# Kernel optimization log

Measured on AMD Instinct MI355X. Metric: run time of the kernel, lower is better.

## Reference

```python
import jax, jax.numpy as jnp
import numpy as np

B, DIM, HEADS, H, W = 4, 192, 6, 256, 256
C = DIM // HEADS  # channels per head
DN = ('NCHW', 'OIHW', 'NCHW')


def conv2d(x, w, b, padding='VALID', groups=1):
    y = jax.lax.conv_general_dilated(x, w, (1, 1), padding,
                                     dimension_numbers=DN,
                                     feature_group_count=groups)
    return y + b[None, :, None, None]


def setup_inputs() -> dict:
    key = jax.random.key(0)
    ks = jax.random.split(key, 8)
    s = 0.02
    return {
        'x': jax.random.normal(ks[0], (B, DIM, H, W), jnp.float32),
        'qkv_w': jax.random.normal(ks[1], (3 * DIM, DIM, 1, 1), jnp.float32) * s,
        'qkv_b': jnp.zeros((3 * DIM,), jnp.float32),
        'dw_w': jax.random.normal(ks[2], (3 * DIM, 1, 3, 3), jnp.float32) * s,
        'dw_b': jnp.zeros((3 * DIM,), jnp.float32),
        'proj_w': jax.random.normal(ks[3], (DIM, DIM, 1, 1), jnp.float32) * s,
        'proj_b': jnp.zeros((DIM,), jnp.float32),
        'temperature': jnp.ones((HEADS, 1, 1, 1), jnp.float32),
    }


def reference(x, qkv_w, qkv_b, dw_w, dw_b, proj_w, proj_b, temperature):
    # qkv projection: 1x1 conv then 3x3 depthwise conv
    qkv = conv2d(x, qkv_w, qkv_b)
    qkv = conv2d(qkv, dw_w, dw_b, padding='SAME', groups=3 * DIM)
    q, k, v = jnp.split(qkv, 3, axis=1)  # each (B, DIM, H, W)

    def heads(t):
        return t.reshape(B, HEADS, C, H, W)
    q, k, v = heads(q), heads(k), heads(v)

    # L2-normalize along W (matches F.normalize eps=1e-12)
    eps = 1e-12
    q = q / jnp.maximum(jnp.linalg.norm(q, axis=-1, keepdims=True), eps)
    k = k / jnp.maximum(jnp.linalg.norm(k, axis=-1, keepdims=True), eps)

    # per-channel HxH attention, contraction over W; temperature broadcasts over head
    attn = jnp.einsum('bncxw,bncyw->bncxy', q, k) * temperature  # (B,HEADS,C,H,H)
    attn = jax.nn.softmax(attn, axis=-1)
    out = jnp.einsum('bncxy,bncyw->bncxw', attn, v)  # (B,HEADS,C,H,W)

    out = out.reshape(B, DIM, H, W)
    return conv2d(out, proj_w, proj_b)
```

## Files before the change

kernel.cpp:

```cpp
#include <hip/hip_runtime.h>
#include <hip/hip_bf16.h>
#include <math.h>


#define HW 65536
#define IMW 256

typedef short bf16x8 __attribute__((ext_vector_type(8)));
typedef float f32x4  __attribute__((ext_vector_type(4)));

__device__ __forceinline__ float bf2f(ushort u) {
    return __uint_as_float((uint)u << 16);
}
__device__ __forceinline__ ushort f2bf(float f) {
    uint i = __float_as_uint(f);
    return (ushort)((i + 0x7FFFu + ((i >> 16) & 1u)) >> 16);
}

__global__ __launch_bounds__(256) void cvt_f32_bf16(const float* __restrict__ s,
                                                    ushort* __restrict__ d, int n)
{
    int i = blockIdx.x * 256 + threadIdx.x;
    if (i < n) d[i] = f2bf(s[i]);
}

__global__ __launch_bounds__(256) void cvt_transpose_f32(const float* __restrict__ src,
                                                         ushort* __restrict__ dst,
                                                         int R, int C,
                                                         long ssS, long ssD)
{
    __shared__ ushort Ls[64][72];
    int t = threadIdx.x;
    long z = blockIdx.z;
    src += z * ssS; dst += z * ssD;
    int c0 = blockIdx.x * 64, r0 = blockIdx.y * 64;
    {
        int r = t >> 2, cs = t & 3;
        const float* gp = src + (size_t)(r0 + r) * C + c0 + cs * 16;
        ushort tmp[16];
        #pragma unroll
        for (int q = 0; q < 4; ++q) {
            float4 v = *(const float4*)(gp + q * 4);
            tmp[q*4+0] = f2bf(v.x); tmp[q*4+1] = f2bf(v.y);
            tmp[q*4+2] = f2bf(v.z); tmp[q*4+3] = f2bf(v.w);
        }
        *(uint4*)&Ls[r][cs * 16]     = *(uint4*)&tmp[0];
        *(uint4*)&Ls[r][cs * 16 + 8] = *(uint4*)&tmp[8];
    }
    __syncthreads();
    {
        int cc = t & 63, seg = t >> 6;
        ushort tmp[16];
        #pragma unroll
        for (int j = 0; j < 16; ++j) tmp[j] = Ls[seg * 16 + j][cc];
        ushort* op = dst + (size_t)(c0 + cc) * R + r0 + seg * 16;
        *(uint4*)(op)     = *(uint4*)&tmp[0];
        *(uint4*)(op + 8) = *(uint4*)&tmp[8];
    }
}

__global__ __launch_bounds__(256) void transpose_bf16(const ushort* __restrict__ src,
                                                      ushort* __restrict__ dst,
                                                      int R, int C,
                                                      long ssS, long ssD)
{
    __shared__ ushort Ls[64][72];
    int t = threadIdx.x;
    long z = blockIdx.z;
    src += z * ssS; dst += z * ssD;
    int c0 = blockIdx.x * 64, r0 = blockIdx.y * 64;
    {
        int r = t >> 2, cs = t & 3;
        const ushort* gp = src + (size_t)(r0 + r) * C + c0 + cs * 16;
        *(uint4*)&Ls[r][cs * 16]     = *(const uint4*)(gp);
        *(uint4*)&Ls[r][cs * 16 + 8] = *(const uint4*)(gp + 8);
    }
    __syncthreads();
    {
        int cc = t & 63, seg = t >> 6;
        ushort tmp[16];
        #pragma unroll
        for (int j = 0; j < 16; ++j) tmp[j] = Ls[seg * 16 + j][cc];
        ushort* op = dst + (size_t)(c0 + cc) * R + r0 + seg * 16;
        *(uint4*)(op)     = *(uint4*)&tmp[0];
        *(uint4*)(op + 8) = *(uint4*)&tmp[8];
    }
}

__global__ __launch_bounds__(256) void transpose_v(const ushort* __restrict__ post,
                                                   ushort* __restrict__ vt)
{
    __shared__ ushort Ls[64][72];
    int t = threadIdx.x;
    int s = blockIdx.z;
    int b = s / 192, r = s - b * 192;
    const ushort* src = post + ((size_t)b * 576 + 384 + r) * HW;
    ushort*       dst = vt + (size_t)s * HW;
    int c0 = blockIdx.x * 64, r0 = blockIdx.y * 64;
    {
        int rr = t >> 2, cs = t & 3;
        const ushort* gp = src + (size_t)(r0 + rr) * IMW + c0 + cs * 16;
        *(uint4*)&Ls[rr][cs * 16]     = *(const uint4*)(gp);
        *(uint4*)&Ls[rr][cs * 16 + 8] = *(const uint4*)(gp + 8);
    }
    __syncthreads();
    {
        int cc = t & 63, seg = t >> 6;
        ushort tmp[16];
        #pragma unroll
        for (int j = 0; j < 16; ++j) tmp[j] = Ls[seg * 16 + j][cc];
        ushort* op = dst + (size_t)(c0 + cc) * IMW + r0 + seg * 16;
        *(uint4*)(op)     = *(uint4*)&tmp[0];
        *(uint4*)(op + 8) = *(uint4*)&tmp[8];
    }
}

__global__ __launch_bounds__(256) void gemm_mfma(const ushort* __restrict__ A, int lda, long sliceA,
                                                 const ushort* __restrict__ B, int ldb, long sliceB,
                                                 void* __restrict__ Dp, int ldd, long sliceD,
                                                 const float* __restrict__ bias,
                                                 int K, int outF32, int NM, int NN)
{
    int lin = blockIdx.x;
    int r8 = lin & 7, kk_ = lin >> 3;
    int m = kk_ % NM, fg = kk_ / NM;
    int g = fg * 8 + r8;
    int nt_ = g % NN;
    long z = g / NN;
    int m0 = m * 64, n0 = nt_ * 256;

    __shared__ ushort Ws[64][40];
    __shared__ ushort Xs[256][40];
    int t = threadIdx.x, wv = t >> 6, lane = t & 63;
    A += z * sliceA; B += z * sliceB;

    f32x4 acc[16];
    #pragma unroll
    for (int i = 0; i < 16; ++i) acc[i] = (f32x4){0.f, 0.f, 0.f, 0.f};

    for (int k0 = 0; k0 < K; k0 += 32) {
        {   int r = t >> 2, s = t & 3;
            *(uint4*)&Ws[r][s * 8] =
                *(const uint4*)(A + (size_t)(m0 + r) * lda + k0 + s * 8);
        }
        {   const ushort* bp = B + (size_t)(n0 + t) * ldb + k0;
            #pragma unroll
            for (int s = 0; s < 4; ++s)
                *(uint4*)&Xs[t][s * 8] = *(const uint4*)(bp + s * 8);
        }
        __syncthreads();
        bf16x8 a = *(const bf16x8*)&Ws[wv * 16 + (lane & 15)][(lane >> 4) * 8];
        #pragma unroll
        for (int nt = 0; nt < 16; ++nt) {
            bf16x8 b = *(const bf16x8*)&Xs[nt * 16 + (lane & 15)][(lane >> 4) * 8];
            acc[nt] = __builtin_amdgcn_mfma_f32_16x16x32_bf16(a, b, acc[nt], 0, 0, 0);
        }
        __syncthreads();
    }

    int mrow = m0 + wv * 16 + (lane >> 4) * 4;
    int ncol = n0 + (lane & 15);
    if (outF32) {
        float* D = (float*)Dp + z * sliceD;
        #pragma unroll
        for (int r_ = 0; r_ < 4; ++r_) {
            float bv = bias ? bias[mrow + r_] : 0.f;
            #pragma unroll
            for (int nt = 0; nt < 16; ++nt)
                D[(size_t)(mrow + r_) * ldd + ncol + nt * 16] = acc[nt][r_] + bv;
        }
    } else {
        ushort* D = (ushort*)Dp + z * sliceD;
        #pragma unroll
        for (int r_ = 0; r_ < 4; ++r_) {
            float bv = bias ? bias[mrow + r_] : 0.f;
            #pragma unroll
            for (int nt = 0; nt < 16; ++nt)
                D[(size_t)(mrow + r_) * ldd + ncol + nt * 16] = f2bf(acc[nt][r_] + bv);
        }
    }
}

__global__ __launch_bounds__(256) void attn_fused(const ushort* __restrict__ post,
                                                  const ushort* __restrict__ vt,
                                                  const float* __restrict__ temp,
                                                  ushort* __restrict__ O)
{
    __shared__ ushort Ws[64][40];
    __shared__ ushort Xs[256][40];
    __shared__ ushort Ps[64][264];
    int t = threadIdx.x, wv = t >> 6, lane = t & 63;
    int lin = blockIdx.x;
    int r8 = lin & 7, k_ = lin >> 3;
    int mtile = k_ & 3, fg = k_ >> 2;
    int s = fg * 8 + r8;
    int b = s / 192, ch = s - b * 192;
    const ushort* Aq = post + ((size_t)b * 576 + ch) * HW;
    const ushort* Bk = Aq + (size_t)192 * HW;
    const ushort* Vt = vt + (size_t)s * HW;
    int m0 = mtile * 64;

    f32x4 acc[16];
    #pragma unroll
    for (int i = 0; i < 16; ++i) acc[i] = (f32x4){0.f, 0.f, 0.f, 0.f};

    for (int k0 = 0; k0 < 256; k0 += 32) {
        {   int r = t >> 2, ss = t & 3;
            *(uint4*)&Ws[r][ss * 8] =
                *(const uint4*)(Aq + (size_t)(m0 + r) * IMW + k0 + ss * 8);
        }
        {   const ushort* bp = Bk + (size_t)t * IMW + k0;
            #pragma unroll
            for (int ss = 0; ss < 4; ++ss)
                *(uint4*)&Xs[t][ss * 8] = *(const uint4*)(bp + ss * 8);
        }
        __syncthreads();
        bf16x8 a = *(const bf16x8*)&Ws[wv * 16 + (lane & 15)][(lane >> 4) * 8];
        #pragma unroll
        for (int nt = 0; nt < 16; ++nt) {
            bf16x8 bfrag = *(const bf16x8*)&Xs[nt * 16 + (lane & 15)][(lane >> 4) * 8];
            acc[nt] = __builtin_amdgcn_mfma_f32_16x16x32_bf16(a, bfrag, acc[nt], 0, 0, 0);
        }
        __syncthreads();
    }

    float tv = temp[ch >> 5];
    #pragma unroll
    for (int r_ = 0; r_ < 4; ++r_) {
        float v[16];
        float mx = -3.4e38f;
        #pragma unroll
        for (int nt = 0; nt < 16; ++nt) { v[nt] = acc[nt][r_] * tv; mx = fmaxf(mx, v[nt]); }
        #pragma unroll
        for (int sh = 1; sh < 16; sh <<= 1) mx = fmaxf(mx, __shfl_xor(mx, sh, 64));
        float sum = 0.f;
        #pragma unroll
        for (int nt = 0; nt < 16; ++nt) { v[nt] = __expf(v[nt] - mx); sum += v[nt]; }
        #pragma unroll
        for (int sh = 1; sh < 16; sh <<= 1) sum += __shfl_xor(sum, sh, 64);
        float inv = 1.f / sum;
        int ml = wv * 16 + (lane >> 4) * 4 + r_;
        #pragma unroll
        for (int nt = 0; nt < 16; ++nt)
            Ps[ml][(lane & 15) + nt * 16] = f2bf(v[nt] * inv);
    }

    f32x4 acc2[16];
    #pragma unroll
    for (int i = 0; i < 16; ++i) acc2[i] = (f32x4){0.f, 0.f, 0.f, 0.f};

    for (int y0 = 0; y0 < 256; y0 += 32) {
        {   const ushort* bp = Vt + (size_t)t * IMW + y0;
            #pragma unroll
            for (int ss = 0; ss < 4; ++ss)
                *(uint4*)&Xs[t][ss * 8] = *(const uint4*)(bp + ss * 8);
        }
        __syncthreads();
        bf16x8 a = *(const bf16x8*)&Ps[wv * 16 + (lane & 15)][y0 + (lane >> 4) * 8];
        #pragma unroll
        for (int nt = 0; nt < 16; ++nt) {
            bf16x8 bfrag = *(const bf16x8*)&Xs[nt * 16 + (lane & 15)][(lane >> 4) * 8];
            acc2[nt] = __builtin_amdgcn_mfma_f32_16x16x32_bf16(a, bfrag, acc2[nt], 0, 0, 0);
        }
        __syncthreads();
    }

    ushort* Op = O + (size_t)s * HW;
    int mrow = m0 + wv * 16 + (lane >> 4) * 4;
    int ncol = lane & 15;
    #pragma unroll
    for (int r_ = 0; r_ < 4; ++r_) {
        #pragma unroll
        for (int nt = 0; nt < 16; ++nt)
            Op[(size_t)(mrow + r_) * IMW + ncol + nt * 16] = f2bf(acc2[nt][r_]);
    }
}

__global__ __launch_bounds__(256) void dw3x3_l2norm(const ushort* __restrict__ in,
                                                    const float* __restrict__ w,
                                                    const float* __restrict__ bias,
                                                    ushort* __restrict__ out)
{
    int t = threadIdx.x;
    int lane = t & 63, wv = t >> 6;
    int ch = blockIdx.y;
    int r0 = blockIdx.x * 16 + wv * 4;
    const ushort* img  = in  + ((size_t)blockIdx.z * 576 + ch) * HW;
    ushort*       outp = out + ((size_t)blockIdx.z * 576 + ch) * HW;
    int px = lane * 4;

    float rv[6][4], lv[6], rx[6];
    #pragma unroll
    for (int i = 0; i < 6; ++i) {
        int rr = r0 - 1 + i;
        if ((unsigned)rr <= 255u) {
            ushort4 cv = *(const ushort4*)&img[(size_t)rr * IMW + px];
            rv[i][0] = bf2f(cv.x); rv[i][1] = bf2f(cv.y);
            rv[i][2] = bf2f(cv.z); rv[i][3] = bf2f(cv.w);
        } else {
            rv[i][0] = rv[i][1] = rv[i][2] = rv[i][3] = 0.f;
        }
        float l = __shfl_up(rv[i][3], 1, 64);
        lv[i] = (lane == 0) ? 0.f : l;
        float r = __shfl_down(rv[i][0], 1, 64);
        rx[i] = (lane == 63) ? 0.f : r;
    }

    const float* wch = w + ch * 9;
    float bv = bias[ch];
    bool do_norm = (ch < 384);

    #pragma unroll
    for (int j = 0; j < 4; ++j) {
        float a0 = bv, a1 = bv, a2 = bv, a3 = bv;
        #pragma unroll
        for (int dy = 0; dy < 3; ++dy) {
            int i = j + dy;
            float w0 = wch[dy * 3], w1 = wch[dy * 3 + 1], w2 = wch[dy * 3 + 2];
            a0 += lv[i]    * w0 + rv[i][0] * w1 + rv[i][1] * w2;
            a1 += rv[i][0] * w0 + rv[i][1] * w1 + rv[i][2] * w2;
            a2 += rv[i][1] * w0 + rv[i][2] * w1 + rv[i][3] * w2;
            a3 += rv[i][2] * w0 + rv[i][3] * w1 + rx[i]    * w2;
        }
        if (do_norm) {
            float ss = a0 * a0 + a1 * a1 + a2 * a2 + a3 * a3;
            #pragma unroll
            for (int m = 1; m < 64; m <<= 1) ss += __shfl_xor(ss, m, 64);
            float inv = 1.0f / fmaxf(sqrtf(ss), 1e-12f);
            a0 *= inv; a1 *= inv; a2 *= inv; a3 *= inv;
        }
        ushort4 o;
        o.x = f2bf(a0); o.y = f2bf(a1); o.z = f2bf(a2); o.w = f2bf(a3);
        *(ushort4*)&outp[(size_t)(r0 + j) * IMW + px] = o;
    }
}

extern "C" void kernel_launch(void* const* d_in, const int* in_sizes, int n_in,
                              void* d_out, int out_size, void* d_ws, size_t ws_size,
                              hipStream_t stream)
{
    const float* x      = (const float*)d_in[0];
    const float* qkv_w  = (const float*)d_in[1];
    const float* qkv_b  = (const float*)d_in[2];
    const float* dw_w   = (const float*)d_in[3];
    const float* dw_b   = (const float*)d_in[4];
    const float* proj_w = (const float*)d_in[5];
    const float* proj_b = (const float*)d_in[6];
    const float* temp   = (const float*)d_in[7];
    float* out = (float*)d_out;

    const size_t off_wq   = 0;
    const size_t off_wp   = 110592;
    const size_t off_pre  = 262144;
    const size_t off_post = off_pre + (size_t)4 * 576 * HW;
    const size_t off_xt   = off_post + (size_t)4 * 576 * HW;
    const size_t total_us = off_xt + (size_t)4 * 192 * HW;
    if (ws_size < total_us * sizeof(ushort)) return;

    ushort* wsb  = (ushort*)d_ws;
    ushort* wq   = wsb + off_wq;
    ushort* wp   = wsb + off_wp;
    ushort* pre  = wsb + off_pre;
    ushort* post = wsb + off_post;
    ushort* xt   = wsb + off_xt;
    ushort* Obuf = pre;
    ushort* Otb  = pre + (size_t)4 * 192 * HW;

    const long SL = (long)192 * HW;

    cvt_f32_bf16<<<dim3(432), 256, 0, stream>>>(qkv_w, wq, 110592);
    cvt_f32_bf16<<<dim3(144), 256, 0, stream>>>(proj_w, wp, 36864);

    cvt_transpose_f32<<<dim3(1024, 3, 4), 256, 0, stream>>>(x, xt, 192, HW, SL, SL);
    gemm_mfma<<<dim3(9 * 256 * 4), 256, 0, stream>>>(wq, 192, 0, xt, 192, SL,
                                                     pre, HW, (long)576 * HW,
                                                     qkv_b, 192, 0, 9, 256);
    dw3x3_l2norm<<<dim3(16, 576, 4), 256, 0, stream>>>(pre, dw_w, dw_b, post);
    transpose_v<<<dim3(4, 4, 768), 256, 0, stream>>>(post, xt);
    attn_fused<<<dim3(4 * 768), 256, 0, stream>>>(post, xt, temp, Obuf);
    transpose_bf16<<<dim3(1024, 3, 4), 256, 0, stream>>>(Obuf, Otb, 192, HW, SL, SL);
    gemm_mfma<<<dim3(3 * 256 * 4), 256, 0, stream>>>(wp, 192, 0, Otb, 192, SL,
                                                     out, HW, SL,
                                                     proj_b, 192, 1, 3, 256);
}
```

Before: 742.4 us.

## Rewrite 1x1-conv GEMM to load MFMA fragments directly from global, 64x64 per wave

The pointwise-conv GEMM drops its shared-memory staging and the two barriers per K step. Each wave now loads its A and B fragments straight from global memory and computes a 64x64 output tile as a 4x4 grid of MFMAs, instead of a 16x256 strip. K is hardcoded to 192 and the loop is partially unrolled. This removes LDS traffic and synchronisation and gives more reuse per register fragment, at the cost of redundant global/L2 loads of the weight tile across waves and more accumulator registers.

New measurement: 822.6 us, median of 2. 10.8% more time.

```diff
diff --git a/kernel.cpp b/kernel.cpp
--- a/kernel.cpp
+++ b/kernel.cpp
@@ -119,7 +119,7 @@
                                                  const ushort* __restrict__ B, int ldb, long sliceB,
                                                  void* __restrict__ Dp, int ldd, long sliceD,
                                                  const float* __restrict__ bias,
-                                                 int K, int outF32, int NM, int NN)
+                                                 int outF32, int NM, int NN)
 {
     int lin = blockIdx.x;
     int r8 = lin & 7, kk_ = lin >> 3;
@@ -127,56 +127,64 @@
     int g = fg * 8 + r8;
     int nt_ = g % NN;
     long z = g / NN;
-    int m0 = m * 64, n0 = nt_ * 256;
-
-    __shared__ ushort Ws[64][40];
-    __shared__ ushort Xs[256][40];
+    int m0 = m * 64;
+
     int t = threadIdx.x, wv = t >> 6, lane = t & 63;
+    int nw0 = nt_ * 256 + wv * 64;
+    int fr = lane & 15, fs = (lane >> 4) * 8;
     A += z * sliceA; B += z * sliceB;
 
-    f32x4 acc[16];
-    #pragma unroll
-    for (int i = 0; i < 16; ++i) acc[i] = (f32x4){0.f, 0.f, 0.f, 0.f};
-
-    for (int k0 = 0; k0 < K; k0 += 32) {
-        {   int r = t >> 2, s = t & 3;
-            *(uint4*)&Ws[r][s * 8] =
-                *(const uint4*)(A + (size_t)(m0 + r) * lda + k0 + s * 8);
-        }
-        {   const ushort* bp = B + (size_t)(n0 + t) * ldb + k0;
-            #pragma unroll
-            for (int s = 0; s < 4; ++s)
-                *(uint4*)&Xs[t][s * 8] = *(const uint4*)(bp + s * 8);
-        }
-        __syncthreads();
-        bf16x8 a = *(const bf16x8*)&Ws[wv * 16 + (lane & 15)][(lane >> 4) * 8];
-        #pragma unroll
-        for (int nt = 0; nt < 16; ++nt) {
-            bf16x8 b = *(const bf16x8*)&Xs[nt * 16 + (lane & 15)][(lane >> 4) * 8];
-            acc[nt] = __builtin_amdgcn_mfma_f32_16x16x32_bf16(a, b, acc[nt], 0, 0, 0);
-        }
-        __syncthreads();
-    }
-
-    int mrow = m0 + wv * 16 + (lane >> 4) * 4;
-    int ncol = n0 + (lane & 15);
+    const ushort* ap = A + (size_t)(m0 + fr) * lda + fs;
+    const ushort* bp = B + (size_t)(nw0 + fr) * ldb + fs;
+
+    f32x4 acc[4][4];
+    #pragma unroll
+    for (int i = 0; i < 4; ++i)
+        #pragma unroll
+        for (int j = 0; j < 4; ++j) acc[i][j] = (f32x4){0.f, 0.f, 0.f, 0.f};
+
+    #pragma unroll 2
+    for (int k0 = 0; k0 < 192; k0 += 32) {
+        bf16x8 a[4], b[4];
+        #pragma unroll
+        for (int i = 0; i < 4; ++i)
+            a[i] = *(const bf16x8*)(ap + (size_t)(i * 16) * lda + k0);
+        #pragma unroll
+        for (int j = 0; j < 4; ++j)
+            b[j] = *(const bf16x8*)(bp + (size_t)(j * 16) * ldb + k0);
+        #pragma unroll
+        for (int i = 0; i < 4; ++i)
+            #pragma unroll
+            for (int j = 0; j < 4; ++j)
+                acc[i][j] = __builtin_amdgcn_mfma_f32_16x16x32_bf16(a[i], b[j], acc[i][j], 0, 0, 0);
+    }
+
+    int rbase = (lane >> 4) * 4;
     if (outF32) {
         float* D = (float*)Dp + z * sliceD;
         #pragma unroll
-        for (int r_ = 0; r_ < 4; ++r_) {
-            float bv = bias ? bias[mrow + r_] : 0.f;
-            #pragma unroll
-            for (int nt = 0; nt < 16; ++nt)
-                D[(size_t)(mrow + r_) * ldd + ncol + nt * 16] = acc[nt][r_] + bv;
+        for (int i = 0; i < 4; ++i) {
+            #pragma unroll
+            for (int r_ = 0; r_ < 4; ++r_) {
+                int mrow = m0 + i * 16 + rbase + r_;
+                float bv = bias ? bias[mrow] : 0.f;
+                #pragma unroll
+                for (int j = 0; j < 4; ++j)
+                    D[(size_t)mrow * ldd + nw0 + j * 16 + fr] = acc[i][j][r_] + bv;
+            }
         }
     } else {
         ushort* D = (ushort*)Dp + z * sliceD;
         #pragma unroll
-        for (int r_ = 0; r_ < 4; ++r_) {
-            float bv = bias ? bias[mrow + r_] : 0.f;
-            #pragma unroll
-            for (int nt = 0; nt < 16; ++nt)
-                D[(size_t)(mrow + r_) * ldd + ncol + nt * 16] = f2bf(acc[nt][r_] + bv);
+        for (int i = 0; i < 4; ++i) {
+            #pragma unroll
+            for (int r_ = 0; r_ < 4; ++r_) {
+                int mrow = m0 + i * 16 + rbase + r_;
+                float bv = bias ? bias[mrow] : 0.f;
+                #pragma unroll
+                for (int j = 0; j < 4; ++j)
+                    D[(size_t)mrow * ldd + nw0 + j * 16 + fr] = f2bf(acc[i][j][r_] + bv);
+            }
         }
     }
 }
@@ -374,12 +382,12 @@
     cvt_transpose_f32<<<dim3(1024, 3, 4), 256, 0, stream>>>(x, xt, 192, HW, SL, SL);
     gemm_mfma<<<dim3(9 * 256 * 4), 256, 0, stream>>>(wq, 192, 0, xt, 192, SL,
                                                      pre, HW, (long)576 * HW,
-                                                     qkv_b, 192, 0, 9, 256);
+                                                     qkv_b, 0, 9, 256);
     dw3x3_l2norm<<<dim3(16, 576, 4), 256, 0, stream>>>(pre, dw_w, dw_b, post);
     transpose_v<<<dim3(4, 4, 768), 256, 0, stream>>>(post, xt);
     attn_fused<<<dim3(4 * 768), 256, 0, stream>>>(post, xt, temp, Obuf);
     transpose_bf16<<<dim3(1024, 3, 4), 256, 0, stream>>>(Obuf, Otb, 192, HW, SL, SL);
     gemm_mfma<<<dim3(3 * 256 * 4), 256, 0, stream>>>(wp, 192, 0, Otb, 192, SL,
                                                      out, HW, SL,
-                                                     proj_b, 192, 1, 3, 256);
-}
+                                                     proj_b, 1, 3, 256);
+}
```
